# Kernel tuning notes

Hardware: AMD Instinct MI355X
Metric: run time of the kernel (lower is better)

## Reference

```python
import jax, jax.numpy as jnp
import numpy as np

B, N, S, K = 8, 16384, 1024, 32
C_STEM, C_PATCH, PE_DIM = 64, 128, 24
RADIUS = 0.2
NUM_BANDS = PE_DIM // 6  # 4 freq bands, sin+cos per xyz axis -> 3*2*4 = 24


def setup_inputs() -> dict:
    key = jax.random.key(0)
    ks = jax.random.split(key, 6)
    xyz = jax.random.uniform(ks[0], (B, N, 3), dtype=jnp.float32)
    point_feature = jax.random.normal(ks[1], (B, N, C_STEM), dtype=jnp.float32)
    patch_center = jax.random.uniform(ks[2], (B, S, 3), dtype=jnp.float32)
    in_dim = C_STEM + 3 + PE_DIM  # grouped_feature + relative_xyz + pos-enc
    w1 = jax.random.normal(ks[3], (in_dim, C_PATCH), dtype=jnp.float32) / np.sqrt(in_dim)
    b1 = jnp.zeros((C_PATCH,), dtype=jnp.float32)
    w2 = jax.random.normal(ks[4], (C_PATCH, C_PATCH), dtype=jnp.float32) / np.sqrt(C_PATCH)
    b2 = jnp.zeros((C_PATCH,), dtype=jnp.float32)
    return dict(xyz=xyz, point_feature=point_feature, patch_center=patch_center,
                w1=w1, b1=b1, w2=w2, b2=b2)


def query_ball_point(radius, nsample, xyz, new_xyz):
    # Standard PointNet++ ball query. xyz:[B,N,3], new_xyz:[B,S,3] -> idx:[B,S,K]
    n = xyz.shape[1]
    sqrdists = jnp.sum((new_xyz[:, :, None, :] - xyz[:, None, :, :]) ** 2, axis=-1)  # [B,S,N]
    gi = jnp.where(sqrdists > radius * radius, n,
                   jnp.arange(n, dtype=jnp.int32)[None, None, :])
    gi = jnp.sort(gi, axis=-1)[:, :, :nsample]           # first K in-ball indices
    first = gi[:, :, :1]
    gi = jnp.where(gi == n, first, gi)                   # pad misses with first hit
    return jnp.minimum(gi, n - 1)


def index_points(points, idx):
    # points:[B,N,C], idx:[B,S,K] -> [B,S,K,C]
    b = points.shape[0]
    return points[jnp.arange(b)[:, None, None], idx]


def pos_encode(rel):
    # NeRF-style sinusoidal encoding of relative xyz: [...,3] -> [...,PE_DIM]
    freqs = (2.0 ** jnp.arange(NUM_BANDS, dtype=jnp.float32)) * jnp.pi
    ang = rel[..., None] * freqs                          # [...,3,NB]
    enc = jnp.concatenate([jnp.sin(ang), jnp.cos(ang)], axis=-1)  # [...,3,2NB]
    return enc.reshape(rel.shape[:-1] + (PE_DIM,))


def reference(xyz, point_feature, patch_center, w1, b1, w2, b2):
    neighbor_idx = query_ball_point(RADIUS, K, xyz, patch_center)   # [B,S,K]
    grouped_xyz = index_points(xyz, neighbor_idx)                    # [B,S,K,3]
    grouped_feature = index_points(point_feature, neighbor_idx)      # [B,S,K,C_STEM]
    relative_xyz = grouped_xyz - patch_center[:, :, None, :]
    relative_position = pos_encode(relative_xyz)                     # [B,S,K,PE_DIM]
    grouped_input = jnp.concatenate(
        (grouped_feature, relative_xyz, relative_position), axis=-1)  # [B,S,K,91]
    h = jax.nn.relu(grouped_input @ w1 + b1)   # PointMLP 1 (shared per-point MLP)
    h = h @ w2 + b2                            # PointMLP 2 (no activation)
    patch_feature = jnp.max(h, axis=2)         # max-pool over K neighbors -> [B,S,C_PATCH]
    return (patch_feature, neighbor_idx)
```

## Files before the change

### kernel.cpp

```cpp
#include <hip/hip_runtime.h>
#include <hip/hip_bf16.h>

#define B_ 8
#define N_ 16384
#define S_ 1024
#define K_ 32
#define CSTEM 64
#define CPATCH 128
#define INDIM 91
#define LDA 104
#define LDH 136
#define PPB 4

typedef __attribute__((ext_vector_type(8))) short short8v;
typedef __attribute__((ext_vector_type(4))) float f32x4;

static __device__ __forceinline__ unsigned short f2bf(float f) {
  union { float f; unsigned int u; } v; v.f = f;
  return (unsigned short)((v.u + 0x7FFFu + ((v.u >> 16) & 1u)) >> 16);
}

__global__ __launch_bounds__(256) void pack_weights(
    const float* __restrict__ w1, const float* __restrict__ w2,
    unsigned short* __restrict__ w1p, unsigned short* __restrict__ w2p)
{
  const int id = blockIdx.x * 256 + threadIdx.x;
  if (id < 3 * 8 * 64) {
    const int l = id & 63, ct = (id >> 6) & 7, ks = id >> 9;
    const int col = 16 * ct + (l & 15);
    const int kb = 32 * ks + (l >> 4) * 8;
    unsigned short v[8];
    #pragma unroll
    for (int j = 0; j < 8; ++j) {
      const int k = kb + j;
      v[j] = (k < INDIM) ? f2bf(w1[k * CPATCH + col]) : (unsigned short)0;
    }
    *(short8v*)&w1p[(size_t)id * 8] = *(const short8v*)v;
  } else if (id < 3 * 8 * 64 + 4 * 8 * 64) {
    const int id2 = id - 3 * 8 * 64;
    const int l = id2 & 63, ct = (id2 >> 6) & 7, ks = id2 >> 9;
    const int col = 16 * ct + (l & 15);
    const int kb = 32 * ks + (l >> 4) * 8;
    unsigned short v[8];
    #pragma unroll
    for (int j = 0; j < 8; ++j) v[j] = f2bf(w2[(kb + j) * CPATCH + col]);
    *(short8v*)&w2p[(size_t)id2 * 8] = *(const short8v*)v;
  }
}

__global__ __launch_bounds__(256, 6) void ball_query_kernel(
    const float* __restrict__ xyz, const float* __restrict__ pc,
    float* __restrict__ idx_out)
{
  const int w    = threadIdx.x >> 6;
  const int lane = threadIdx.x & 63;
  const int bs   = blockIdx.x * 4 + w;
  const int b    = bs >> 10;

  const float* __restrict__ xb = xyz + (size_t)b * N_ * 3;
  const double cx = (double)pc[bs * 3 + 0];
  const double cy = (double)pc[bs * 3 + 1];
  const double cz = (double)pc[bs * 3 + 2];
  const double rr = 0.2 * 0.2;

  __shared__ int fidx[4][K_];

  const unsigned long long lower = (1ull << lane) - 1ull;
  const int lo3 = lane * 12;
  int found = 0;
  int base = 0;

  float4 c0 = *(const float4*)&xb[lo3 + 0];
  float4 c1 = *(const float4*)&xb[lo3 + 4];
  float4 c2 = *(const float4*)&xb[lo3 + 8];

  for (;;) {
    const bool last = (base + 256 >= N_);
    const int pb = last ? base : base + 256;
    const float4 n0 = *(const float4*)&xb[pb * 3 + lo3 + 0];
    const float4 n1 = *(const float4*)&xb[pb * 3 + lo3 + 4];
    const float4 n2 = *(const float4*)&xb[pb * 3 + lo3 + 8];

    const int i0 = base + lane * 4;
    double dx, dy, dz;
    dx = (double)c0.x - cx; dy = (double)c0.y - cy; dz = (double)c0.z - cz;
    const bool in0 = (dx * dx + dy * dy + dz * dz) <= rr;
    dx = (double)c0.w - cx; dy = (double)c1.x - cy; dz = (double)c1.y - cz;
    const bool in1 = (dx * dx + dy * dy + dz * dz) <= rr;
    dx = (double)c1.z - cx; dy = (double)c1.w - cy; dz = (double)c2.x - cz;
    const bool in2 = (dx * dx + dy * dy + dz * dz) <= rr;
    dx = (double)c2.y - cx; dy = (double)c2.z - cy; dz = (double)c2.w - cz;
    const bool in3 = (dx * dx + dy * dy + dz * dz) <= rr;

    const unsigned long long b0 = __ballot(in0);
    const unsigned long long b1 = __ballot(in1);
    const unsigned long long b2 = __ballot(in2);
    const unsigned long long b3 = __ballot(in3);

    int p = found + __popcll(b0 & lower) + __popcll(b1 & lower)
                  + __popcll(b2 & lower) + __popcll(b3 & lower);
    if (in0) { if (p < K_) fidx[w][p] = i0 + 0; ++p; }
    if (in1) { if (p < K_) fidx[w][p] = i0 + 1; ++p; }
    if (in2) { if (p < K_) fidx[w][p] = i0 + 2; ++p; }
    if (in3) { if (p < K_) fidx[w][p] = i0 + 3; }

    found += __popcll(b0) + __popcll(b1) + __popcll(b2) + __popcll(b3);
    if (found >= K_ || last) break;
    base += 256;
    c0 = n0; c1 = n1; c2 = n2;
  }
  __threadfence_block();
  if (lane < K_) {
    const int fill = (found == 0) ? (N_ - 1) : fidx[w][0];
    const int v = (lane < found) ? fidx[w][lane] : fill;
    idx_out[(size_t)bs * K_ + lane] = (float)v;
  }
}

__global__ __launch_bounds__(256, 2) void patch_mlp_mfma(
    const float* __restrict__ xyz, const float* __restrict__ pf,
    const float* __restrict__ pc,
    const unsigned short* __restrict__ w1p, const float* __restrict__ b1,
    const unsigned short* __restrict__ w2p, const float* __restrict__ b2,
    const float* __restrict__ idx_f, float* __restrict__ out)
{
  const int tid  = threadIdx.x;
  const int lane = tid & 63;
  const int w    = tid >> 6;

  __shared__ int sidx[K_];
  __shared__ float scen[3];
  __shared__ __align__(16) unsigned short As[K_][LDA];
  __shared__ __align__(16) unsigned short Hs[K_][LDH];

  short8v w1f[3][2], w2f[4][2];
  #pragma unroll
  for (int ks = 0; ks < 3; ++ks)
    #pragma unroll
    for (int t = 0; t < 2; ++t)
      w1f[ks][t] = *(const short8v*)&w1p[((size_t)(ks * 8 + 2 * w + t) * 64 + lane) * 8];
  #pragma unroll
  for (int ks = 0; ks < 4; ++ks)
    #pragma unroll
    for (int t = 0; t < 2; ++t)
      w2f[ks][t] = *(const short8v*)&w2p[((size_t)(ks * 8 + 2 * w + t) * 64 + lane) * 8];

  const float bias1[2] = { b1[32 * w + (lane & 15)], b1[32 * w + 16 + (lane & 15)] };
  const float bias2[2] = { b2[32 * w + (lane & 15)], b2[32 * w + 16 + (lane & 15)] };

  for (int p = 0; p < PPB; ++p) {
    const int bs = blockIdx.x * PPB + p;
    const int b  = bs >> 10;
    const float* __restrict__ pfb = pf  + (size_t)b * N_ * CSTEM;
    const float* __restrict__ xb  = xyz + (size_t)b * N_ * 3;

    if (tid < K_) sidx[tid] = (int)idx_f[(size_t)bs * K_ + tid];
    if (tid < 3)  scen[tid] = pc[bs * 3 + tid];
    __syncthreads();

    {
      const int row = tid >> 3, sub = tid & 7;
      const int r = sidx[row];
      const float4 f0 = *(const float4*)&pfb[(size_t)r * CSTEM + sub * 8];
      const float4 f1 = *(const float4*)&pfb[(size_t)r * CSTEM + sub * 8 + 4];
      unsigned short v[8];
      v[0] = f2bf(f0.x); v[1] = f2bf(f0.y); v[2] = f2bf(f0.z); v[3] = f2bf(f0.w);
      v[4] = f2bf(f1.x); v[5] = f2bf(f1.y); v[6] = f2bf(f1.z); v[7] = f2bf(f1.w);
      *(short8v*)&As[row][sub * 8] = *(const short8v*)v;
    }
    {
      const int row = tid & 31, j = tid >> 5;
      const int r = sidx[row];
      float rel[3];
      rel[0] = xb[r * 3 + 0] - scen[0];
      rel[1] = xb[r * 3 + 1] - scen[1];
      rel[2] = xb[r * 3 + 2] - scen[2];
      #pragma unroll
      for (int cc = 0; cc < 4; ++cc) {
        const int c = 64 + 4 * j + cc;
        float val;
        if (c < 67) val = rel[c - 64];
        else if (c < 91) {
          const int q = c - 67, d = q >> 3, rbit = q & 7, band = rbit & 3;
          const float ang = rel[d] * ((float)(1 << band) * 3.14159265358979323846f);
          val = (rbit < 4) ? sinf(ang) : cosf(ang);
        } else val = 0.f;
        As[row][c] = f2bf(val);
      }
    }
    __syncthreads();

    f32x4 acc[2][2] = {};
    #pragma unroll
    for (int ks = 0; ks < 3; ++ks) {
      const int k0 = ks * 32 + (lane >> 4) * 8;
      const short8v a0 = *(const short8v*)&As[(lane & 15)][k0];
      const short8v a1 = *(const short8v*)&As[16 + (lane & 15)][k0];
      acc[0][0] = __builtin_amdgcn_mfma_f32_16x16x32_bf16(a0, w1f[ks][0], acc[0][0], 0, 0, 0);
      acc[0][1] = __builtin_amdgcn_mfma_f32_16x16x32_bf16(a0, w1f[ks][1], acc[0][1], 0, 0, 0);
      acc[1][0] = __builtin_amdgcn_mfma_f32_16x16x32_bf16(a1, w1f[ks][0], acc[1][0], 0, 0, 0);
      acc[1][1] = __builtin_amdgcn_mfma_f32_16x16x32_bf16(a1, w1f[ks][1], acc[1][1], 0, 0, 0);
    }
    #pragma unroll
    for (int rt = 0; rt < 2; ++rt)
      #pragma unroll
      for (int t = 0; t < 2; ++t)
        #pragma unroll
        for (int reg = 0; reg < 4; ++reg) {
          const float h = fmaxf(acc[rt][t][reg] + bias1[t], 0.f);
          const int row = 16 * rt + (lane >> 4) * 4 + reg;
          const int col = 32 * w + 16 * t + (lane & 15);
          Hs[row][col] = f2bf(h);
        }
    __syncthreads();

    f32x4 acc2[2][2] = {};
    #pragma unroll
    for (int ks = 0; ks < 4; ++ks) {
      const int k0 = ks * 32 + (lane >> 4) * 8;
      const short8v a0 = *(const short8v*)&Hs[(lane & 15)][k0];
      const short8v a1 = *(const short8v*)&Hs[16 + (lane & 15)][k0];
      acc2[0][0] = __builtin_amdgcn_mfma_f32_16x16x32_bf16(a0, w2f[ks][0], acc2[0][0], 0, 0, 0);
      acc2[0][1] = __builtin_amdgcn_mfma_f32_16x16x32_bf16(a0, w2f[ks][1], acc2[0][1], 0, 0, 0);
      acc2[1][0] = __builtin_amdgcn_mfma_f32_16x16x32_bf16(a1, w2f[ks][0], acc2[1][0], 0, 0, 0);
      acc2[1][1] = __builtin_amdgcn_mfma_f32_16x16x32_bf16(a1, w2f[ks][1], acc2[1][1], 0, 0, 0);
    }
    float m0 = -3.4e38f, m1 = -3.4e38f;
    #pragma unroll
    for (int rt = 0; rt < 2; ++rt)
      #pragma unroll
      for (int reg = 0; reg < 4; ++reg) {
        m0 = fmaxf(m0, acc2[rt][0][reg]);
        m1 = fmaxf(m1, acc2[rt][1][reg]);
      }
    m0 += bias2[0];
    m1 += bias2[1];
    m0 = fmaxf(m0, __shfl_xor(m0, 16));
    m0 = fmaxf(m0, __shfl_xor(m0, 32));
    m1 = fmaxf(m1, __shfl_xor(m1, 16));
    m1 = fmaxf(m1, __shfl_xor(m1, 32));
    if (lane < 16) {
      out[(size_t)bs * CPATCH + 32 * w + lane]      = m0;
      out[(size_t)bs * CPATCH + 32 * w + 16 + lane] = m1;
    }
    __syncthreads();
  }
}

extern "C" void kernel_launch(void* const* d_in, const int* in_sizes, int n_in,
                              void* d_out, int out_size, void* d_ws, size_t ws_size,
                              hipStream_t stream) {
  const float* xyz = (const float*)d_in[0];
  const float* pf  = (const float*)d_in[1];
  const float* pc  = (const float*)d_in[2];
  const float* w1  = (const float*)d_in[3];
  const float* b1  = (const float*)d_in[4];
  const float* w2  = (const float*)d_in[5];
  const float* b2  = (const float*)d_in[6];

  float* out     = (float*)d_out;
  float* idx_out = out + (size_t)B_ * S_ * CPATCH;

  unsigned short* w1p = (unsigned short*)d_ws;
  unsigned short* w2p = w1p + 96 * 128;

  pack_weights<<<14, 256, 0, stream>>>(w1, w2, w1p, w2p);
  ball_query_kernel<<<B_ * S_ / 4, 256, 0, stream>>>(xyz, pc, idx_out);
  patch_mlp_mfma<<<B_ * S_ / PPB, 256, 0, stream>>>(xyz, pf, pc, w1p, b1, w2p, b2,
                                                    idx_out, out);
}
```

Baseline: 54.04 us.

## Fuse ball query into patch MLP kernel with block-wide scan

Removes the separate ball-query kernel and performs the radius search inside the patch MLP block. All four waves scan 1024 points per iteration and combine per-wave counts through shared memory. The selected neighbor coordinates are kept in shared memory, so the relative xyz no longer has to be gathered from global memory. This saves one launch and the index write/read round trip. In exchange it adds two block barriers per scan step, and the MLP block can run only two blocks per CU during the search phase.

```diff
diff --git a/kernel.cpp b/kernel.cpp
--- a/kernel.cpp
+++ b/kernel.cpp
@@ -48,88 +48,20 @@
   }
 }
 
-__global__ __launch_bounds__(256, 6) void ball_query_kernel(
-    const float* __restrict__ xyz, const float* __restrict__ pc,
-    float* __restrict__ idx_out)
-{
-  const int w    = threadIdx.x >> 6;
-  const int lane = threadIdx.x & 63;
-  const int bs   = blockIdx.x * 4 + w;
-  const int b    = bs >> 10;
-
-  const float* __restrict__ xb = xyz + (size_t)b * N_ * 3;
-  const double cx = (double)pc[bs * 3 + 0];
-  const double cy = (double)pc[bs * 3 + 1];
-  const double cz = (double)pc[bs * 3 + 2];
-  const double rr = 0.2 * 0.2;
-
-  __shared__ int fidx[4][K_];
-
-  const unsigned long long lower = (1ull << lane) - 1ull;
-  const int lo3 = lane * 12;
-  int found = 0;
-  int base = 0;
-
-  float4 c0 = *(const float4*)&xb[lo3 + 0];
-  float4 c1 = *(const float4*)&xb[lo3 + 4];
-  float4 c2 = *(const float4*)&xb[lo3 + 8];
-
-  for (;;) {
-    const bool last = (base + 256 >= N_);
-    const int pb = last ? base : base + 256;
-    const float4 n0 = *(const float4*)&xb[pb * 3 + lo3 + 0];
-    const float4 n1 = *(const float4*)&xb[pb * 3 + lo3 + 4];
-    const float4 n2 = *(const float4*)&xb[pb * 3 + lo3 + 8];
-
-    const int i0 = base + lane * 4;
-    double dx, dy, dz;
-    dx = (double)c0.x - cx; dy = (double)c0.y - cy; dz = (double)c0.z - cz;
-    const bool in0 = (dx * dx + dy * dy + dz * dz) <= rr;
-    dx = (double)c0.w - cx; dy = (double)c1.x - cy; dz = (double)c1.y - cz;
-    const bool in1 = (dx * dx + dy * dy + dz * dz) <= rr;
-    dx = (double)c1.z - cx; dy = (double)c1.w - cy; dz = (double)c2.x - cz;
-    const bool in2 = (dx * dx + dy * dy + dz * dz) <= rr;
-    dx = (double)c2.y - cx; dy = (double)c2.z - cy; dz = (double)c2.w - cz;
-    const bool in3 = (dx * dx + dy * dy + dz * dz) <= rr;
-
-    const unsigned long long b0 = __ballot(in0);
-    const unsigned long long b1 = __ballot(in1);
-    const unsigned long long b2 = __ballot(in2);
-    const unsigned long long b3 = __ballot(in3);
-
-    int p = found + __popcll(b0 & lower) + __popcll(b1 & lower)
-                  + __popcll(b2 & lower) + __popcll(b3 & lower);
-    if (in0) { if (p < K_) fidx[w][p] = i0 + 0; ++p; }
-    if (in1) { if (p < K_) fidx[w][p] = i0 + 1; ++p; }
-    if (in2) { if (p < K_) fidx[w][p] = i0 + 2; ++p; }
-    if (in3) { if (p < K_) fidx[w][p] = i0 + 3; }
-
-    found += __popcll(b0) + __popcll(b1) + __popcll(b2) + __popcll(b3);
-    if (found >= K_ || last) break;
-    base += 256;
-    c0 = n0; c1 = n1; c2 = n2;
-  }
-  __threadfence_block();
-  if (lane < K_) {
-    const int fill = (found == 0) ? (N_ - 1) : fidx[w][0];
-    const int v = (lane < found) ? fidx[w][lane] : fill;
-    idx_out[(size_t)bs * K_ + lane] = (float)v;
-  }
-}
-
-__global__ __launch_bounds__(256, 2) void patch_mlp_mfma(
+__global__ __launch_bounds__(256, 2) void fused_patch(
     const float* __restrict__ xyz, const float* __restrict__ pf,
     const float* __restrict__ pc,
     const unsigned short* __restrict__ w1p, const float* __restrict__ b1,
     const unsigned short* __restrict__ w2p, const float* __restrict__ b2,
-    const float* __restrict__ idx_f, float* __restrict__ out)
+    float* __restrict__ idx_out, float* __restrict__ out)
 {
   const int tid  = threadIdx.x;
   const int lane = tid & 63;
   const int w    = tid >> 6;
 
-  __shared__ int sidx[K_];
-  __shared__ float scen[3];
+  __shared__ int   sidx[K_];
+  __shared__ float sxyz[K_][3];
+  __shared__ int   scnt[4];
   __shared__ __align__(16) unsigned short As[K_][LDA];
   __shared__ __align__(16) unsigned short Hs[K_][LDH];
 
@@ -148,15 +80,80 @@
   const float bias1[2] = { b1[32 * w + (lane & 15)], b1[32 * w + 16 + (lane & 15)] };
   const float bias2[2] = { b2[32 * w + (lane & 15)], b2[32 * w + 16 + (lane & 15)] };
 
+  const unsigned long long lower = (1ull << lane) - 1ull;
+  const int off = (w << 8) + (lane << 2);
+
   for (int p = 0; p < PPB; ++p) {
     const int bs = blockIdx.x * PPB + p;
     const int b  = bs >> 10;
+    const float* __restrict__ xb  = xyz + (size_t)b * N_ * 3;
     const float* __restrict__ pfb = pf  + (size_t)b * N_ * CSTEM;
-    const float* __restrict__ xb  = xyz + (size_t)b * N_ * 3;
-
-    if (tid < K_) sidx[tid] = (int)idx_f[(size_t)bs * K_ + tid];
-    if (tid < 3)  scen[tid] = pc[bs * 3 + tid];
-    __syncthreads();
+
+    const float cen0 = pc[bs * 3 + 0];
+    const float cen1 = pc[bs * 3 + 1];
+    const float cen2 = pc[bs * 3 + 2];
+    const double cx = (double)cen0, cy = (double)cen1, cz = (double)cen2;
+    const double rr = 0.2 * 0.2;
+
+    int found = 0;
+    for (int base = 0; base < N_; base += 1024) {
+      const int i0 = base + off;
+      const float4 p0 = *(const float4*)&xb[i0 * 3 + 0];
+      const float4 p1 = *(const float4*)&xb[i0 * 3 + 4];
+      const float4 p2 = *(const float4*)&xb[i0 * 3 + 8];
+
+      double dx, dy, dz;
+      dx = (double)p0.x - cx; dy = (double)p0.y - cy; dz = (double)p0.z - cz;
+      const bool in0 = (dx * dx + dy * dy + dz * dz) <= rr;
+      dx = (double)p0.w - cx; dy = (double)p1.x - cy; dz = (double)p1.y - cz;
+      const bool in1 = (dx * dx + dy * dy + dz * dz) <= rr;
+      dx = (double)p1.z - cx; dy = (double)p1.w - cy; dz = (double)p2.x - cz;
+      const bool in2 = (dx * dx + dy * dy + dz * dz) <= rr;
+      dx = (double)p2.y - cx; dy = (double)p2.z - cy; dz = (double)p2.w - cz;
+      const bool in3 = (dx * dx + dy * dy + dz * dz) <= rr;
+
+      const unsigned long long m0 = __ballot(in0);
+      const unsigned long long m1 = __ballot(in1);
+      const unsigned long long m2 = __ballot(in2);
+      const unsigned long long m3 = __ballot(in3);
+
+      if (lane == 0)
+        scnt[w] = __popcll(m0) + __popcll(m1) + __popcll(m2) + __popcll(m3);
+      __syncthreads();
+
+      int pre = found;
+      #pragma unroll
+      for (int v = 0; v < 4; ++v) if (v < w) pre += scnt[v];
+      const int tot = scnt[0] + scnt[1] + scnt[2] + scnt[3];
+
+      int pp = pre + __popcll(m0 & lower) + __popcll(m1 & lower)
+                   + __popcll(m2 & lower) + __popcll(m3 & lower);
+      if (in0) { if (pp < K_) { sidx[pp] = i0;     sxyz[pp][0] = p0.x; sxyz[pp][1] = p0.y; sxyz[pp][2] = p0.z; } ++pp; }
+      if (in1) { if (pp < K_) { sidx[pp] = i0 + 1; sxyz[pp][0] = p0.w; sxyz[pp][1] = p1.x; sxyz[pp][2] = p1.y; } ++pp; }
+      if (in2) { if (pp < K_) { sidx[pp] = i0 + 2; sxyz[pp][0] = p1.z; sxyz[pp][1] = p1.w; sxyz[pp][2] = p2.x; } ++pp; }
+      if (in3) { if (pp < K_) { sidx[pp] = i0 + 3; sxyz[pp][0] = p2.y; sxyz[pp][1] = p2.z; sxyz[pp][2] = p2.w; } }
+
+      found += tot;
+      __syncthreads();
+      if (found >= K_) break;
+    }
+
+    if (found == 0 && tid == 0) {
+      sidx[0] = N_ - 1;
+      sxyz[0][0] = xb[(N_ - 1) * 3 + 0];
+      sxyz[0][1] = xb[(N_ - 1) * 3 + 1];
+      sxyz[0][2] = xb[(N_ - 1) * 3 + 2];
+    }
+    __syncthreads();
+    if (tid > 0 && tid >= found && tid < K_) {
+      sidx[tid] = sidx[0];
+      sxyz[tid][0] = sxyz[0][0];
+      sxyz[tid][1] = sxyz[0][1];
+      sxyz[tid][2] = sxyz[0][2];
+    }
+    __syncthreads();
+
+    if (tid < K_) idx_out[(size_t)bs * K_ + tid] = (float)sidx[tid];
 
     {
       const int row = tid >> 3, sub = tid & 7;
@@ -170,11 +167,10 @@
     }
     {
       const int row = tid & 31, j = tid >> 5;
-      const int r = sidx[row];
       float rel[3];
-      rel[0] = xb[r * 3 + 0] - scen[0];
-      rel[1] = xb[r * 3 + 1] - scen[1];
-      rel[2] = xb[r * 3 + 2] - scen[2];
+      rel[0] = sxyz[row][0] - cen0;
+      rel[1] = sxyz[row][1] - cen1;
+      rel[2] = sxyz[row][2] - cen2;
       #pragma unroll
       for (int cc = 0; cc < 4; ++cc) {
         const int c = 64 + 4 * j + cc;
@@ -265,7 +261,6 @@
   unsigned short* w2p = w1p + 96 * 128;
 
   pack_weights<<<14, 256, 0, stream>>>(w1, w2, w1p, w2p);
-  ball_query_kernel<<<B_ * S_ / 4, 256, 0, stream>>>(xyz, pc, idx_out);
-  patch_mlp_mfma<<<B_ * S_ / PPB, 256, 0, stream>>>(xyz, pf, pc, w1p, b1, w2p, b2,
-                                                    idx_out, out);
-}
+  fused_patch<<<B_ * S_ / PPB, 256, 0, stream>>>(xyz, pf, pc, w1p, b1, w2p, b2,
+                                                 idx_out, out);
+}
```

Result: slower. 61.84 us (+14.4%).
